# Kernel optimization log

Measured on AMD Instinct MI355X. Metric: run time of the kernel, lower is better.

The kernel has to match this reference:

```python
import jax, jax.numpy as jnp
import numpy as np

D_MODEL = 1024
D_K = 1024
D_V = 1024
N_HEAD = 16
EPS = 1e-5
BS, N_TOK = 2, 2048


def setup_inputs() -> dict:
    key = jax.random.key(0)
    ks = jax.random.split(key, 12)
    s = 0.02
    q = jax.random.normal(ks[0], (BS, N_TOK, D_MODEL), jnp.float32)
    k = jax.random.normal(ks[1], (BS, N_TOK, D_MODEL), jnp.float32)
    v = jax.random.normal(ks[2], (BS, N_TOK, D_MODEL), jnp.float32)
    return {
        "q": q, "k": k, "v": v,
        "gamma": jnp.ones((D_MODEL,), jnp.float32),
        "beta": jnp.zeros((D_MODEL,), jnp.float32),
        "Wq": jax.random.normal(ks[3], (D_MODEL, D_K), jnp.float32) * s,
        "bq": jnp.zeros((D_K,), jnp.float32),
        "Wk": jax.random.normal(ks[4], (D_MODEL, D_K), jnp.float32) * s,
        "bk": jnp.zeros((D_K,), jnp.float32),
        "Wv": jax.random.normal(ks[5], (D_MODEL, D_V), jnp.float32) * s,
        "bv": jnp.zeros((D_V,), jnp.float32),
        "Wo": jax.random.normal(ks[6], (D_V, D_MODEL), jnp.float32) * s,
        "bo": jnp.zeros((D_MODEL,), jnp.float32),
    }


def reference(q, k, v, gamma, beta, Wq, bq, Wk, bk, Wv, bv, Wo, bo):
    # NOTE: original module ignores k, v args; self-attention over q.
    bs, n_tok, d_m = q.shape
    d_h = D_K // N_HEAD
    temper = float(np.sqrt(d_h))

    # LayerNorm1d over d_model
    mu = jnp.mean(q, axis=-1, keepdims=True)
    var = jnp.var(q, axis=-1, keepdims=True)
    h = (q - mu) / jnp.sqrt(var + EPS) * gamma + beta

    # projections; head split = chunk along feature dim -> [bs, H, T, d_h]
    qh = (h @ Wq + bq).reshape(bs, n_tok, N_HEAD, d_h).transpose(0, 2, 1, 3)
    kh = (h @ Wk + bk).reshape(bs, n_tok, N_HEAD, d_h).transpose(0, 2, 1, 3)
    vh = jax.nn.relu(h @ Wv + bv).reshape(bs, n_tok, N_HEAD, d_h).transpose(0, 2, 1, 3)

    scores = jnp.einsum('bhqd,bhkd->bhqk', qh, kh) / temper
    # dropout before softmax in train mode; identity in eval (deterministic ref)
    attn = jax.nn.softmax(scores, axis=-1)
    o = jnp.einsum('bhqk,bhkd->bhqd', attn, vh)  # [bs, H, T, d_h]

    # faithful to torch: view(bs, n_tok, -1) with NO head transpose (head-major merge)
    merged = o.reshape(bs, n_tok, N_HEAD * d_h)
    out = merged @ Wo + bo + q  # proj + residual
    return out
```

## Files before the change

### kernel.cpp

```cpp
#include <hip/hip_runtime.h>

typedef __bf16 bf16;
typedef __bf16 bf16x8 __attribute__((ext_vector_type(8)));
typedef __bf16 bf16x4 __attribute__((ext_vector_type(4)));
typedef float  f32x4  __attribute__((ext_vector_type(4)));
typedef unsigned int u32;
typedef u32 u32x4 __attribute__((ext_vector_type(4)));

#define AS1U(p) ((const __attribute__((address_space(1))) unsigned int*)(p))
#define AS3U(p) ((__attribute__((address_space(3))) unsigned int*)(p))

static __device__ __forceinline__ u32 pack2(float a, float b) {
    unsigned short ua = __builtin_bit_cast(unsigned short, (bf16)a);
    unsigned short ub = __builtin_bit_cast(unsigned short, (bf16)b);
    return (u32)ua | ((u32)ub << 16);
}

__global__ void transpose_cast4_kernel(const float* __restrict__ W0, const float* __restrict__ W1,
                                       const float* __restrict__ W2, const float* __restrict__ W3,
                                       bf16* __restrict__ D0, bf16* __restrict__ D1,
                                       bf16* __restrict__ D2, bf16* __restrict__ D3) {
    __shared__ float tile[32][33];
    const float* W; bf16* D;
    switch (blockIdx.z) {
        case 0: W = W0; D = D0; break;
        case 1: W = W1; D = D1; break;
        case 2: W = W2; D = D2; break;
        default: W = W3; D = D3; break;
    }
    const int bj = blockIdx.x, bi = blockIdx.y;
    const int tx = threadIdx.x, ty = threadIdx.y;
#pragma unroll
    for (int i = 0; i < 4; i++) {
        tile[ty + i * 8][tx] = W[(size_t)(bi * 32 + ty + i * 8) * 1024 + bj * 32 + tx];
    }
    __syncthreads();
#pragma unroll
    for (int i = 0; i < 4; i++) {
        D[(size_t)(bj * 32 + ty + i * 8) * 1024 + bi * 32 + tx] =
            (bf16)tile[tx][ty + i * 8];
    }
}

__global__ void layernorm_kernel(const float* __restrict__ x,
                                 const float* __restrict__ gamma,
                                 const float* __restrict__ beta,
                                 bf16* __restrict__ h) {
    const int row = blockIdx.x;
    const float* xr = x + (size_t)row * 1024;
    const int t = threadIdx.x;
    float4 v = ((const float4*)xr)[t];
    float s  = v.x + v.y + v.z + v.w;
    float s2 = v.x * v.x + v.y * v.y + v.z * v.z + v.w * v.w;
#pragma unroll
    for (int m = 1; m < 64; m <<= 1) {
        s  += __shfl_xor(s, m, 64);
        s2 += __shfl_xor(s2, m, 64);
    }
    __shared__ float ssum[4], ssum2[4];
    const int wid = t >> 6, lane = t & 63;
    if (lane == 0) { ssum[wid] = s; ssum2[wid] = s2; }
    __syncthreads();
    s  = ssum[0] + ssum[1] + ssum[2] + ssum[3];
    s2 = ssum2[0] + ssum2[1] + ssum2[2] + ssum2[3];
    const float mu  = s * (1.f / 1024.f);
    const float var = s2 * (1.f / 1024.f) - mu * mu;
    const float rs  = rsqrtf(var + 1e-5f);
    float4 g = ((const float4*)gamma)[t];
    float4 b = ((const float4*)beta)[t];
    bf16x4 o;
    o[0] = (bf16)((v.x - mu) * rs * g.x + b.x);
    o[1] = (bf16)((v.y - mu) * rs * g.y + b.y);
    o[2] = (bf16)((v.z - mu) * rs * g.z + b.z);
    o[3] = (bf16)((v.w - mu) * rs * g.w + b.w);
    ((bf16x4*)(h + (size_t)row * 1024))[t] = o;
}

template <int EPI>
__global__ void gemm_kernel(const bf16* __restrict__ A, const bf16* __restrict__ BT,
                            int N, int K,
                            bf16* __restrict__ Cb,
                            const float* __restrict__ b0, const float* __restrict__ b1,
                            const float* __restrict__ b2, bf16* __restrict__ Vt,
                            float* __restrict__ Cf, const float* __restrict__ bo,
                            const float* __restrict__ resid) {
    __shared__ bf16 Asm[128][32];
    __shared__ bf16 Bsm[128][32];
    const int tid = threadIdx.x;
    const int lane = tid & 63, wave = tid >> 6;
    const int wr = wave >> 1, wc = wave & 1;
    const int tileN = blockIdx.x * 128, tileM = blockIdx.y * 128;
    const int row16 = lane & 15, g = lane >> 4;

    f32x4 acc[4][4] = {};

    for (int kt = 0; kt < K; kt += 32) {
#pragma unroll
        for (int i = 0; i < 2; i++) {
            int c = tid + i * 256;
            int r = c >> 2, cb = (c & 3) * 16;
            const char* g_ = (const char*)(A + (size_t)(tileM + r) * K + kt) + cb;
            char* l_ = (char*)&Asm[0][0] + c * 16;
            __builtin_amdgcn_global_load_lds(AS1U(g_), AS3U(l_), 16, 0, 0);
        }
#pragma unroll
        for (int i = 0; i < 2; i++) {
            int c = tid + i * 256;
            int r = c >> 2, cb = (c & 3) * 16;
            const char* g_ = (const char*)(BT + (size_t)(tileN + r) * K + kt) + cb;
            char* l_ = (char*)&Bsm[0][0] + c * 16;
            __builtin_amdgcn_global_load_lds(AS1U(g_), AS3U(l_), 16, 0, 0);
        }
        __syncthreads();
        bf16x8 af[4], bfr[4];
#pragma unroll
        for (int m = 0; m < 4; m++)
            af[m] = *(const bf16x8*)&Asm[wr * 64 + m * 16 + row16][g * 8];
#pragma unroll
        for (int n = 0; n < 4; n++)
            bfr[n] = *(const bf16x8*)&Bsm[wc * 64 + n * 16 + row16][g * 8];
#pragma unroll
        for (int m = 0; m < 4; m++)
#pragma unroll
            for (int n = 0; n < 4; n++)
                acc[m][n] = __builtin_amdgcn_mfma_f32_16x16x32_bf16(af[m], bfr[n],
                                                                   acc[m][n], 0, 0, 0);
        __syncthreads();
    }
#pragma unroll
    for (int m = 0; m < 4; m++) {
        const int row = tileM + wr * 64 + m * 16 + g * 4;
#pragma unroll
        for (int n = 0; n < 4; n++) {
            const int col = tileN + wc * 64 + n * 16 + row16;
            if (EPI == 0 && col >= 2048) {
                const int d = col - 2048;
                const float bias = b2[d];
                bf16x4 pk;
#pragma unroll
                for (int j = 0; j < 4; j++) {
                    float v = acc[m][n][j] + bias;
                    pk[j] = (bf16)fmaxf(v, 0.f);
                }
                const int bb = row >> 11, tt = row & 2047;
                const int hh = d >> 6, dd = d & 63;
                *(bf16x4*)&Vt[(((size_t)bb * 16 + hh) * 64 + dd) * 2048 + tt] = pk;
            } else {
#pragma unroll
                for (int j = 0; j < 4; j++) {
                    float v = acc[m][n][j];
                    const int r = row + j;
                    if (EPI == 0) {
                        if (col < 1024) {
                            v = (v + b0[col]) * 0.18033688011112042f;
                        } else {
                            v += b1[col - 1024];
                        }
                        Cb[(size_t)r * N + col] = (bf16)v;
                    } else {
                        v += bo[col] + resid[(size_t)r * N + col];
                        Cf[(size_t)r * N + col] = v;
                    }
                }
            }
        }
    }
}

__global__ __launch_bounds__(256, 4)
void attn_kernel(const bf16* __restrict__ qkv, const bf16* __restrict__ Vt,
                 bf16* __restrict__ Obuf) {
    const int bid = blockIdx.x;
    const int swz = (bid & 7) * 128 + (bid >> 3);
    const int bh = swz >> 5, qt = swz & 31;
    const int b = bh >> 4, h = bh & 15;
    const int qbase = qt * 64;
    const int tid = threadIdx.x;
    const int lane = tid & 63, wv = tid >> 6;
    const int row16 = lane & 15, g = lane >> 4;

    __shared__ bf16 Kl[2][64][64];
    __shared__ bf16 Vl[2][64][64];

    const bf16* qrow = qkv + (size_t)(b * 2048 + qbase + wv * 16 + row16) * 3072 + h * 64;
    const bf16x8 qf0 = *(const bf16x8*)(qrow + g * 8);
    const bf16x8 qf1 = *(const bf16x8*)(qrow + 32 + g * 8);

    const char* kgbase = (const char*)(qkv + (size_t)b * 2048 * 3072 + 1024 + h * 64);
    const char* vgbase = (const char*)(Vt + (size_t)bh * 64 * 2048);
    const int c0 = tid, c1 = tid + 256;
    const int sr0 = c0 >> 3, sc0 = ((c0 & 7) * 16) ^ ((sr0 & 7) << 4);
    const int sr1 = c1 >> 3, sc1 = ((c1 & 7) * 16) ^ ((sr1 & 7) << 4);
    const char* kgp0 = kgbase + (size_t)sr0 * 6144 + sc0;
    const char* kgp1 = kgbase + (size_t)sr1 * 6144 + sc1;
    const char* vgp0 = vgbase + (size_t)sr0 * 4096 + sc0;
    const char* vgp1 = vgbase + (size_t)sr1 * 4096 + sc1;
    char* kld0 = (char*)&Kl[0][0][0] + c0 * 16;
    char* kld1 = (char*)&Kl[0][0][0] + c1 * 16;
    char* vld0 = (char*)&Vl[0][0][0] + c0 * 16;
    char* vld1 = (char*)&Vl[0][0][0] + c1 * 16;

    __builtin_amdgcn_global_load_lds(AS1U(kgp0), AS3U(kld0), 16, 0, 0);
    __builtin_amdgcn_global_load_lds(AS1U(kgp1), AS3U(kld1), 16, 0, 0);
    __builtin_amdgcn_global_load_lds(AS1U(vgp0), AS3U(vld0), 16, 0, 0);
    __builtin_amdgcn_global_load_lds(AS1U(vgp1), AS3U(vld1), 16, 0, 0);

    f32x4 accO[4] = {};
    float l_r = 0.f;

    const int swx = (row16 & 7) << 4;
    const int cx0 = (g * 16) ^ swx;
    const int cx1 = (64 + g * 16) ^ swx;
    const int rbase = row16 * 128;
    const int srcA = (row16 + ((g & 1) << 5)) << 2;
    const int srcB = srcA + 64;
    const bool hi2 = g >= 2;
    const int jb = g << 2;

    for (int t = 0; t < 32; ++t) {
        __syncthreads();
        const int cur = t & 1;
        if (t < 31) {
            const int nb = ((t + 1) & 1) * 8192;
            const size_t ko = (size_t)(t + 1) * 64 * 6144;
            const size_t vo = (size_t)(t + 1) * 128;
            __builtin_amdgcn_global_load_lds(AS1U(kgp0 + ko), AS3U(kld0 + nb), 16, 0, 0);
            __builtin_amdgcn_global_load_lds(AS1U(kgp1 + ko), AS3U(kld1 + nb), 16, 0, 0);
            __builtin_amdgcn_global_load_lds(AS1U(vgp0 + vo), AS3U(vld0 + nb), 16, 0, 0);
            __builtin_amdgcn_global_load_lds(AS1U(vgp1 + vo), AS3U(vld1 + nb), 16, 0, 0);
        }
        const char* Kb = (const char*)&Kl[cur][0][0];
        const char* Vb = (const char*)&Vl[cur][0][0];

        f32x4 accT[4];
#pragma unroll
        for (int n = 0; n < 4; n++) {
            const bf16x8 kf0 = *(const bf16x8*)(Kb + n * 2048 + rbase + cx0);
            const bf16x8 kf1 = *(const bf16x8*)(Kb + n * 2048 + rbase + cx1);
            f32x4 z = {};
            z = __builtin_amdgcn_mfma_f32_16x16x32_bf16(kf0, qf0, z, 0, 0, 0);
            accT[n] = __builtin_amdgcn_mfma_f32_16x16x32_bf16(kf1, qf1, z, 0, 0, 0);
        }

        float sv[16];
        float rs0 = 0.f, rs1 = 0.f;
#pragma unroll
        for (int n = 0; n < 4; n++)
#pragma unroll
            for (int j = 0; j < 4; j++) {
                const float pv = exp2f(accT[n][j]);
                sv[n * 4 + j] = pv;
                if (n & 1) rs1 += pv; else rs0 += pv;
            }
        l_r += rs0 + rs1;

        u32 pk01[4], pk23[4];
#pragma unroll
        for (int n = 0; n < 4; n++) {
            pk01[n] = pack2(sv[n * 4 + 0], sv[n * 4 + 1]);
            pk23[n] = pack2(sv[n * 4 + 2], sv[n * 4 + 3]);
        }

#pragma unroll
        for (int kk = 0; kk < 2; kk++) {
            const int n0 = kk * 2;
            const int w0a = __builtin_amdgcn_ds_bpermute(srcA, (int)pk01[n0]);
            const int w0b = __builtin_amdgcn_ds_bpermute(srcA, (int)pk01[n0 + 1]);
            const int w1a = __builtin_amdgcn_ds_bpermute(srcA, (int)pk23[n0]);
            const int w1b = __builtin_amdgcn_ds_bpermute(srcA, (int)pk23[n0 + 1]);
            const int w2a = __builtin_amdgcn_ds_bpermute(srcB, (int)pk01[n0]);
            const int w2b = __builtin_amdgcn_ds_bpermute(srcB, (int)pk01[n0 + 1]);
            const int w3a = __builtin_amdgcn_ds_bpermute(srcB, (int)pk23[n0]);
            const int w3b = __builtin_amdgcn_ds_bpermute(srcB, (int)pk23[n0 + 1]);
            u32x4 ww;
            ww[0] = (u32)(hi2 ? w0b : w0a);
            ww[1] = (u32)(hi2 ? w1b : w1a);
            ww[2] = (u32)(hi2 ? w2b : w2a);
            ww[3] = (u32)(hi2 ? w3b : w3a);
            const bf16x8 af = __builtin_bit_cast(bf16x8, ww);
            const int cx = kk ? cx1 : cx0;
#pragma unroll
            for (int n = 0; n < 4; n++) {
                const bf16x8 vf = *(const bf16x8*)(Vb + n * 2048 + rbase + cx);
                accO[n] = __builtin_amdgcn_mfma_f32_16x16x32_bf16(af, vf, accO[n], 0, 0, 0);
            }
        }
    }

    l_r += __shfl_xor(l_r, 16);
    l_r += __shfl_xor(l_r, 32);
    const float linv = 1.f / l_r;
    float li[4];
#pragma unroll
    for (int j = 0; j < 4; j++) li[j] = __shfl(linv, jb + j);
    bf16* ob = Obuf + ((size_t)bh * 2048 + qbase + wv * 16) * 64;
#pragma unroll
    for (int n = 0; n < 4; n++)
#pragma unroll
        for (int j = 0; j < 4; j++)
            ob[(size_t)(g * 4 + j) * 64 + n * 16 + row16] = (bf16)(accO[n][j] * li[j]);
}

extern "C" void kernel_launch(void* const* d_in, const int* in_sizes, int n_in,
                              void* d_out, int out_size, void* d_ws, size_t ws_size,
                              hipStream_t stream) {
    const float* q     = (const float*)d_in[0];
    const float* gamma = (const float*)d_in[3];
    const float* beta  = (const float*)d_in[4];
    const float* Wq    = (const float*)d_in[5];
    const float* bq    = (const float*)d_in[6];
    const float* Wk    = (const float*)d_in[7];
    const float* bk    = (const float*)d_in[8];
    const float* Wv    = (const float*)d_in[9];
    const float* bv    = (const float*)d_in[10];
    const float* Wo    = (const float*)d_in[11];
    const float* bo    = (const float*)d_in[12];
    float* out = (float*)d_out;

    char* ws = (char*)d_ws;
    bf16* h     = (bf16*)(ws);
    bf16* WcatT = (bf16*)(ws + (8u << 20));
    bf16* WoT   = (bf16*)(ws + (14u << 20));
    bf16* qkv   = (bf16*)(ws + (16u << 20));
    bf16* Obuf  = (bf16*)(ws + (40u << 20));
    bf16* Vtb   = (bf16*)(ws + (48u << 20));

    transpose_cast4_kernel<<<dim3(32, 32, 4), dim3(32, 8), 0, stream>>>(
        Wq, Wk, Wv, Wo,
        WcatT, WcatT + (size_t)1024 * 1024, WcatT + (size_t)2048 * 1024, WoT);

    layernorm_kernel<<<4096, 256, 0, stream>>>(q, gamma, beta, h);

    gemm_kernel<0><<<dim3(24, 32), 256, 0, stream>>>(h, WcatT, 3072, 1024,
                                                     qkv, bq, bk, bv, Vtb,
                                                     nullptr, nullptr, nullptr);

    attn_kernel<<<1024, 256, 0, stream>>>(qkv, Vtb, Obuf);

    gemm_kernel<1><<<dim3(8, 32), 256, 0, stream>>>(Obuf, WoT, 1024, 1024,
                                                    nullptr, nullptr, nullptr, nullptr, nullptr,
                                                    out, bo, q);
}
```

Baseline: 154.9 us.

## Use 32x32x16 MFMA in attention with 2 waves and permlane32 swap

```diff
diff --git a/kernel.cpp b/kernel.cpp
--- a/kernel.cpp
+++ b/kernel.cpp
@@ -4,6 +4,7 @@
 typedef __bf16 bf16x8 __attribute__((ext_vector_type(8)));
 typedef __bf16 bf16x4 __attribute__((ext_vector_type(4)));
 typedef float  f32x4  __attribute__((ext_vector_type(4)));
+typedef float  f32x16 __attribute__((ext_vector_type(16)));
 typedef unsigned int u32;
 typedef u32 u32x4 __attribute__((ext_vector_type(4)));
 
@@ -167,7 +168,7 @@
     }
 }
 
-__global__ __launch_bounds__(256, 4)
+__global__ __launch_bounds__(128, 2)
 void attn_kernel(const bf16* __restrict__ qkv, const bf16* __restrict__ Vt,
                  bf16* __restrict__ Obuf) {
     const int bid = blockIdx.x;
@@ -177,45 +178,39 @@
     const int qbase = qt * 64;
     const int tid = threadIdx.x;
     const int lane = tid & 63, wv = tid >> 6;
-    const int row16 = lane & 15, g = lane >> 4;
+    const int c = lane & 31, p = lane >> 5;
 
     __shared__ bf16 Kl[2][64][64];
     __shared__ bf16 Vl[2][64][64];
 
-    const bf16* qrow = qkv + (size_t)(b * 2048 + qbase + wv * 16 + row16) * 3072 + h * 64;
-    const bf16x8 qf0 = *(const bf16x8*)(qrow + g * 8);
-    const bf16x8 qf1 = *(const bf16x8*)(qrow + 32 + g * 8);
+    const bf16* qrow = qkv + (size_t)(b * 2048 + qbase + wv * 32 + c) * 3072 + h * 64;
+    bf16x8 qf[4];
+#pragma unroll
+    for (int ch = 0; ch < 4; ch++)
+        qf[ch] = *(const bf16x8*)(qrow + ch * 16 + p * 8);
 
     const char* kgbase = (const char*)(qkv + (size_t)b * 2048 * 3072 + 1024 + h * 64);
     const char* vgbase = (const char*)(Vt + (size_t)bh * 64 * 2048);
-    const int c0 = tid, c1 = tid + 256;
-    const int sr0 = c0 >> 3, sc0 = ((c0 & 7) * 16) ^ ((sr0 & 7) << 4);
-    const int sr1 = c1 >> 3, sc1 = ((c1 & 7) * 16) ^ ((sr1 & 7) << 4);
-    const char* kgp0 = kgbase + (size_t)sr0 * 6144 + sc0;
-    const char* kgp1 = kgbase + (size_t)sr1 * 6144 + sc1;
-    const char* vgp0 = vgbase + (size_t)sr0 * 4096 + sc0;
-    const char* vgp1 = vgbase + (size_t)sr1 * 4096 + sc1;
-    char* kld0 = (char*)&Kl[0][0][0] + c0 * 16;
-    char* kld1 = (char*)&Kl[0][0][0] + c1 * 16;
-    char* vld0 = (char*)&Vl[0][0][0] + c0 * 16;
-    char* vld1 = (char*)&Vl[0][0][0] + c1 * 16;
-
-    __builtin_amdgcn_global_load_lds(AS1U(kgp0), AS3U(kld0), 16, 0, 0);
-    __builtin_amdgcn_global_load_lds(AS1U(kgp1), AS3U(kld1), 16, 0, 0);
-    __builtin_amdgcn_global_load_lds(AS1U(vgp0), AS3U(vld0), 16, 0, 0);
-    __builtin_amdgcn_global_load_lds(AS1U(vgp1), AS3U(vld1), 16, 0, 0);
-
-    f32x4 accO[4] = {};
+    int kgo[4], vgo[4];
+#pragma unroll
+    for (int i = 0; i < 4; i++) {
+        const int cc = tid + i * 128;
+        const int srow = cc >> 3;
+        const int scol = ((cc & 7) * 16) ^ ((srow & 7) << 4);
+        kgo[i] = srow * 6144 + scol;
+        vgo[i] = srow * 4096 + scol;
+    }
+
+#pragma unroll
+    for (int i = 0; i < 4; i++) {
+        __builtin_amdgcn_global_load_lds(AS1U(kgbase + kgo[i]),
+                                         AS3U((char*)&Kl[0][0][0] + (tid + i * 128) * 16), 16, 0, 0);
+        __builtin_amdgcn_global_load_lds(AS1U(vgbase + vgo[i]),
+                                         AS3U((char*)&Vl[0][0][0] + (tid + i * 128) * 16), 16, 0, 0);
+    }
+
+    f32x16 accO[2] = {};
     float l_r = 0.f;
-
-    const int swx = (row16 & 7) << 4;
-    const int cx0 = (g * 16) ^ swx;
-    const int cx1 = (64 + g * 16) ^ swx;
-    const int rbase = row16 * 128;
-    const int srcA = (row16 + ((g & 1) << 5)) << 2;
-    const int srcB = srcA + 64;
-    const bool hi2 = g >= 2;
-    const int jb = g << 2;
 
     for (int t = 0; t < 32; ++t) {
         __syncthreads();
@@ -224,81 +219,74 @@
             const int nb = ((t + 1) & 1) * 8192;
             const size_t ko = (size_t)(t + 1) * 64 * 6144;
             const size_t vo = (size_t)(t + 1) * 128;
-            __builtin_amdgcn_global_load_lds(AS1U(kgp0 + ko), AS3U(kld0 + nb), 16, 0, 0);
-            __builtin_amdgcn_global_load_lds(AS1U(kgp1 + ko), AS3U(kld1 + nb), 16, 0, 0);
-            __builtin_amdgcn_global_load_lds(AS1U(vgp0 + vo), AS3U(vld0 + nb), 16, 0, 0);
-            __builtin_amdgcn_global_load_lds(AS1U(vgp1 + vo), AS3U(vld1 + nb), 16, 0, 0);
+#pragma unroll
+            for (int i = 0; i < 4; i++) {
+                __builtin_amdgcn_global_load_lds(AS1U(kgbase + ko + kgo[i]),
+                                                 AS3U((char*)&Kl[0][0][0] + nb + (tid + i * 128) * 16), 16, 0, 0);
+                __builtin_amdgcn_global_load_lds(AS1U(vgbase + vo + vgo[i]),
+                                                 AS3U((char*)&Vl[0][0][0] + nb + (tid + i * 128) * 16), 16, 0, 0);
+            }
         }
         const char* Kb = (const char*)&Kl[cur][0][0];
         const char* Vb = (const char*)&Vl[cur][0][0];
 
-        f32x4 accT[4];
-#pragma unroll
-        for (int n = 0; n < 4; n++) {
-            const bf16x8 kf0 = *(const bf16x8*)(Kb + n * 2048 + rbase + cx0);
-            const bf16x8 kf1 = *(const bf16x8*)(Kb + n * 2048 + rbase + cx1);
-            f32x4 z = {};
-            z = __builtin_amdgcn_mfma_f32_16x16x32_bf16(kf0, qf0, z, 0, 0, 0);
-            accT[n] = __builtin_amdgcn_mfma_f32_16x16x32_bf16(kf1, qf1, z, 0, 0, 0);
-        }
-
-        float sv[16];
-        float rs0 = 0.f, rs1 = 0.f;
-#pragma unroll
-        for (int n = 0; n < 4; n++)
-#pragma unroll
-            for (int j = 0; j < 4; j++) {
-                const float pv = exp2f(accT[n][j]);
-                sv[n * 4 + j] = pv;
-                if (n & 1) rs1 += pv; else rs0 += pv;
-            }
-        l_r += rs0 + rs1;
-
-        u32 pk01[4], pk23[4];
-#pragma unroll
-        for (int n = 0; n < 4; n++) {
-            pk01[n] = pack2(sv[n * 4 + 0], sv[n * 4 + 1]);
-            pk23[n] = pack2(sv[n * 4 + 2], sv[n * 4 + 3]);
-        }
-
-#pragma unroll
-        for (int kk = 0; kk < 2; kk++) {
-            const int n0 = kk * 2;
-            const int w0a = __builtin_amdgcn_ds_bpermute(srcA, (int)pk01[n0]);
-            const int w0b = __builtin_amdgcn_ds_bpermute(srcA, (int)pk01[n0 + 1]);
-            const int w1a = __builtin_amdgcn_ds_bpermute(srcA, (int)pk23[n0]);
-            const int w1b = __builtin_amdgcn_ds_bpermute(srcA, (int)pk23[n0 + 1]);
-            const int w2a = __builtin_amdgcn_ds_bpermute(srcB, (int)pk01[n0]);
-            const int w2b = __builtin_amdgcn_ds_bpermute(srcB, (int)pk01[n0 + 1]);
-            const int w3a = __builtin_amdgcn_ds_bpermute(srcB, (int)pk23[n0]);
-            const int w3b = __builtin_amdgcn_ds_bpermute(srcB, (int)pk23[n0 + 1]);
-            u32x4 ww;
-            ww[0] = (u32)(hi2 ? w0b : w0a);
-            ww[1] = (u32)(hi2 ? w1b : w1a);
-            ww[2] = (u32)(hi2 ? w2b : w2a);
-            ww[3] = (u32)(hi2 ? w3b : w3a);
-            const bf16x8 af = __builtin_bit_cast(bf16x8, ww);
-            const int cx = kk ? cx1 : cx0;
-#pragma unroll
-            for (int n = 0; n < 4; n++) {
-                const bf16x8 vf = *(const bf16x8*)(Vb + n * 2048 + rbase + cx);
-                accO[n] = __builtin_amdgcn_mfma_f32_16x16x32_bf16(af, vf, accO[n], 0, 0, 0);
-            }
-        }
-    }
-
-    l_r += __shfl_xor(l_r, 16);
+#pragma unroll
+        for (int cc = 0; cc < 2; cc++) {
+            f32x16 accT = {};
+#pragma unroll
+            for (int ch = 0; ch < 4; ch++) {
+                const int tok = cc * 32 + c;
+                const bf16x8 kf = *(const bf16x8*)(Kb + tok * 128 +
+                                                   ((ch * 32 + p * 16) ^ ((tok & 7) << 4)));
+                accT = __builtin_amdgcn_mfma_f32_32x32x16_bf16(kf, qf[ch], accT, 0, 0, 0);
+            }
+            float pv[16];
+            float s = 0.f;
+#pragma unroll
+            for (int r = 0; r < 16; r++) {
+                pv[r] = exp2f(accT[r]);
+                s += pv[r];
+            }
+            l_r += s;
+            u32 k01 = pack2(pv[0], pv[1]),  k23 = pack2(pv[2], pv[3]);
+            u32 k45 = pack2(pv[4], pv[5]),  k67 = pack2(pv[6], pv[7]);
+            u32 k89 = pack2(pv[8], pv[9]),  kab = pack2(pv[10], pv[11]);
+            u32 kcd = pack2(pv[12], pv[13]), kef = pack2(pv[14], pv[15]);
+            asm("v_permlane32_swap_b32 %0, %1" : "+v"(k45), "+v"(k01));
+            asm("v_permlane32_swap_b32 %0, %1" : "+v"(k67), "+v"(k23));
+            asm("v_permlane32_swap_b32 %0, %1" : "+v"(kcd), "+v"(k89));
+            asm("v_permlane32_swap_b32 %0, %1" : "+v"(kef), "+v"(kab));
+            u32x4 w0w = {k01, k23, k45, k67};
+            u32x4 w1w = {k89, kab, kcd, kef};
+            const bf16x8 pf0 = __builtin_bit_cast(bf16x8, w0w);
+            const bf16x8 pf1 = __builtin_bit_cast(bf16x8, w1w);
+#pragma unroll
+            for (int dc = 0; dc < 2; dc++) {
+                const int rd = dc * 32 + c;
+                const int tb0 = (cc * 64 + p * 16) ^ ((rd & 7) << 4);
+                const int tb1 = (cc * 64 + 32 + p * 16) ^ ((rd & 7) << 4);
+                const bf16x8 vf0 = *(const bf16x8*)(Vb + rd * 128 + tb0);
+                const bf16x8 vf1 = *(const bf16x8*)(Vb + rd * 128 + tb1);
+                accO[dc] = __builtin_amdgcn_mfma_f32_32x32x16_bf16(pf0, vf0, accO[dc], 0, 0, 0);
+                accO[dc] = __builtin_amdgcn_mfma_f32_32x32x16_bf16(pf1, vf1, accO[dc], 0, 0, 0);
+            }
+        }
+    }
+
     l_r += __shfl_xor(l_r, 32);
     const float linv = 1.f / l_r;
-    float li[4];
-#pragma unroll
-    for (int j = 0; j < 4; j++) li[j] = __shfl(linv, jb + j);
-    bf16* ob = Obuf + ((size_t)bh * 2048 + qbase + wv * 16) * 64;
-#pragma unroll
-    for (int n = 0; n < 4; n++)
-#pragma unroll
-        for (int j = 0; j < 4; j++)
-            ob[(size_t)(g * 4 + j) * 64 + n * 16 + row16] = (bf16)(accO[n][j] * li[j]);
+    float li[16];
+#pragma unroll
+    for (int r = 0; r < 16; r++)
+        li[r] = __shfl(linv, (r & 3) + 8 * (r >> 2) + 4 * p);
+    bf16* ob = Obuf + ((size_t)bh * 2048 + qbase + wv * 32) * 64;
+#pragma unroll
+    for (int dc = 0; dc < 2; dc++)
+#pragma unroll
+        for (int r = 0; r < 16; r++) {
+            const int row = (r & 3) + 8 * (r >> 2) + 4 * p;
+            ob[(size_t)row * 64 + dc * 32 + c] = (bf16)(accO[dc][r] * li[r]);
+        }
 }
 
 extern "C" void kernel_launch(void* const* d_in, const int* in_sizes, int n_in,
@@ -335,7 +323,7 @@
                                                      qkv, bq, bk, bv, Vtb,
                                                      nullptr, nullptr, nullptr);
 
-    attn_kernel<<<1024, 256, 0, stream>>>(qkv, Vtb, Obuf);
+    attn_kernel<<<1024, 128, 0, stream>>>(qkv, Vtb, Obuf);
 
     gemm_kernel<1><<<dim3(8, 32), 256, 0, stream>>>(Obuf, WoT, 1024, 1024,
                                                     nullptr, nullptr, nullptr, nullptr, nullptr,
```

After: 158.3 us. +2.2%, slower.
